# Optimization experiments

Measured on AMD Instinct MI355X. Metric: run time of the kernel, lower is better.

Reference implementation:

```python
import jax, jax.numpy as jnp
import numpy as np

B, T, C = 4, 2048, 1024
NQ, D = 8, C // 8  # n_query heads, head dim = n_embd // 8


def setup_inputs() -> dict:
    key = jax.random.key(0)
    ks = jax.random.split(key, 6)
    s = 0.02
    return {
        "x": jax.random.normal(ks[0], (B, T, C), dtype=jnp.float32),
        "Wk": jax.random.normal(ks[1], (C, D), dtype=jnp.float32) * s,
        "Wv": jax.random.normal(ks[2], (C, D), dtype=jnp.float32) * s,
        "Wq": jax.random.normal(ks[3], (NQ, C, D), dtype=jnp.float32) * s,
        "Wp": jax.random.normal(ks[4], (NQ * D, C), dtype=jnp.float32) * s,
        "bp": jnp.zeros((C,), dtype=jnp.float32),
    }


def reference(x, Wk, Wv, Wq, Wp, bp):
    b, t, c = x.shape
    scale = c ** -0.5  # original scales by n_embd**-0.5, not head-dim
    k = x @ Wk                                   # [B,T,D] shared across heads (MQA)
    v = x @ Wv                                   # [B,T,D]
    q = jnp.einsum("btc,qcd->bqtd", x, Wq)       # [B,NQ,T,D]
    wei = jnp.einsum("bqtd,bsd->bqts", q, k) * scale
    causal = jnp.tril(jnp.ones((t, t), dtype=bool))
    wei = jnp.where(causal, wei, -jnp.inf)
    wei = jax.nn.softmax(wei, axis=-1)
    out = jnp.einsum("bqts,bsd->btqd", wei, v)   # [B,T,NQ,D]
    out = out.reshape(b, t, -1)                  # concat heads -> [B,T,NQ*D]
    return out @ Wp + bp
```

## Files before the change

kernel.cpp:

```cpp
#include <hip/hip_runtime.h>
#include <hip/hip_bf16.h>
#include <cstddef>
#include <cstdint>

#define B 4
#define T 2048
#define C 1024
#define NQ 8
#define D 128
#define M_ROWS (B * T)
#define NTOT (2 * D + NQ * D)

typedef __bf16 bf16x8 __attribute__((ext_vector_type(8)));
typedef float  f32x4  __attribute__((ext_vector_type(4)));

__device__ __forceinline__ ushort f2bf(float f) {
    union { float f; uint32_t u; } v; v.f = f;
    const uint32_t r = (v.u + 0x7fffu + ((v.u >> 16) & 1u)) >> 16;
    return (ushort)r;
}

__device__ __forceinline__ void gld_lds16(const ushort* g, ushort* lds_uniform) {
    __builtin_amdgcn_global_load_lds(
        (const __attribute__((address_space(1))) void*)g,
        (__attribute__((address_space(3))) void*)lds_uniform, 16, 0, 0);
}

__global__ __launch_bounds__(256) void xcvt(const float* __restrict__ x,
                                            ushort* __restrict__ xb) {
    const size_t i = ((size_t)blockIdx.x * 256 + threadIdx.x) * 8;
    const float4 a = *(const float4*)(x + i);
    const float4 b = *(const float4*)(x + i + 4);
    uint4 o;
    o.x = f2bf(a.x) | ((uint32_t)f2bf(a.y) << 16);
    o.y = f2bf(a.z) | ((uint32_t)f2bf(a.w) << 16);
    o.z = f2bf(b.x) | ((uint32_t)f2bf(b.y) << 16);
    o.w = f2bf(b.z) | ((uint32_t)f2bf(b.w) << 16);
    *(uint4*)(xb + i) = o;
}

__device__ __forceinline__ void wtrans_body(const float* __restrict__ src,
                                            ushort* __restrict__ dst, int NC,
                                            int bx, int by) {
    __shared__ ushort Ts[64][72];
    const int tid = threadIdx.x;
    const int k0 = by * 64, c0 = bx * 64;
    {
        const int r = tid >> 2, cq = tid & 3;
#pragma unroll
        for (int i = 0; i < 4; ++i) {
            const int cc = cq * 16 + i * 4;
            const float4 v = *(const float4*)(src + (size_t)(k0 + r) * NC + c0 + cc);
            uint2 o;
            o.x = f2bf(v.x) | ((uint32_t)f2bf(v.y) << 16);
            o.y = f2bf(v.z) | ((uint32_t)f2bf(v.w) << 16);
            *(uint2*)(&Ts[r][cc]) = o;
        }
    }
    __syncthreads();
    {
        const int n = tid >> 2, kq = tid & 3;
        ushort vv[16];
#pragma unroll
        for (int j = 0; j < 16; ++j) vv[j] = Ts[kq * 16 + j][n];
        uint4 o0, o1;
        o0.x = vv[0] | ((uint32_t)vv[1] << 16);  o0.y = vv[2] | ((uint32_t)vv[3] << 16);
        o0.z = vv[4] | ((uint32_t)vv[5] << 16);  o0.w = vv[6] | ((uint32_t)vv[7] << 16);
        o1.x = vv[8] | ((uint32_t)vv[9] << 16);  o1.y = vv[10] | ((uint32_t)vv[11] << 16);
        o1.z = vv[12] | ((uint32_t)vv[13] << 16); o1.w = vv[14] | ((uint32_t)vv[15] << 16);
        ushort* d = dst + (size_t)(c0 + n) * C + k0 + kq * 16;
        *(uint4*)d = o0;
        *(uint4*)(d + 8) = o1;
    }
}

__global__ __launch_bounds__(256) void wtrans_qkv(const float* __restrict__ Wk,
                                                  const float* __restrict__ Wv,
                                                  const float* __restrict__ Wq,
                                                  ushort* __restrict__ WcatT) {
    const int z = blockIdx.z;
    const float* src;
    int rbase;
    if (z == 0)      { src = Wk; rbase = 0; }
    else if (z == 1) { src = Wv; rbase = D; }
    else             { src = Wq + (size_t)(z - 2) * C * D; rbase = 2 * D + (z - 2) * D; }
    wtrans_body(src, WcatT + (size_t)rbase * C, D, blockIdx.x, blockIdx.y);
}

__global__ __launch_bounds__(256) void wtrans_p(const float* __restrict__ Wp,
                                                ushort* __restrict__ WpT) {
    wtrans_body(Wp, WpT, C, blockIdx.x, blockIdx.y);
}

__global__ __launch_bounds__(256) void vtrans(const ushort* __restrict__ qkv,
                                              ushort* __restrict__ vbT) {
    __shared__ ushort Ts[64][136];
    const int tid = threadIdx.x;
    const int kb0 = blockIdx.x * 64;
    {
        const int r = tid >> 2, cq = tid & 3;
        const ushort* src = qkv + (size_t)(kb0 + r) * NTOT + D;
#pragma unroll
        for (int i = 0; i < 4; ++i) {
            const int cc = (cq * 4 + i) * 8;
            *(uint4*)(&Ts[r][cc]) = *(const uint4*)(src + cc);
        }
    }
    __syncthreads();
    {
        const int d = tid >> 1, half = tid & 1;
        ushort vv[32];
#pragma unroll
        for (int k = 0; k < 32; ++k) vv[k] = Ts[half * 32 + k][d];
        uint32_t dw[16];
#pragma unroll
        for (int i = 0; i < 16; ++i) dw[i] = vv[i] | ((uint32_t)vv[16 + i] << 16);
        uint32_t* dst = (uint32_t*)(vbT + (size_t)d * M_ROWS + kb0 + half * 32);
#pragma unroll
        for (int i = 0; i < 4; ++i)
            *(uint4*)(dst + i * 4) = *(uint4*)(&dw[i * 4]);
    }
}

template <bool BF16_OUT>
__global__ __launch_bounds__(256) void gemm_mfma(const ushort* __restrict__ A,
                                                 const ushort* __restrict__ Bt,
                                                 void* __restrict__ Cout,
                                                 const float* __restrict__ bias,
                                                 const int Nout) {
    __shared__ ushort As[128 * 32];
    __shared__ ushort Bs[128 * 32];
    const int tid  = threadIdx.x;
    const int lane = tid & 63;
    const int w    = tid >> 6;
    const int col  = lane & 15;
    const int quad = lane >> 4;
    const int row0 = blockIdx.y * 128;
    const int col0 = blockIdx.x * 128;
    const int wm = w & 1, wn = w >> 1;

    const int srow = lane >> 2;
    const int skk  = (lane & 3) * 8;

    f32x4 acc[4][4];
#pragma unroll
    for (int i = 0; i < 4; ++i)
#pragma unroll
        for (int j = 0; j < 4; ++j) acc[i][j] = (f32x4){0.f, 0.f, 0.f, 0.f};

    for (int k0 = 0; k0 < C; k0 += 32) {
        __syncthreads();
#pragma unroll
        for (int j = 0; j < 2; ++j) {
            const int ci = w * 2 + j;
            const int r  = ci * 16 + srow;
            gld_lds16(A  + (size_t)(row0 + r) * C + k0 + skk, &As[ci * 512]);
            gld_lds16(Bt + (size_t)(col0 + r) * C + k0 + skk, &Bs[ci * 512]);
        }
        __syncthreads();

        bf16x8 af[4], bfr[4];
#pragma unroll
        for (int i = 0; i < 4; ++i)
            af[i] = *(const bf16x8*)&As[(wm * 64 + i * 16 + col) * 32 + quad * 8];
#pragma unroll
        for (int j = 0; j < 4; ++j)
            bfr[j] = *(const bf16x8*)&Bs[(wn * 64 + j * 16 + col) * 32 + quad * 8];
#pragma unroll
        for (int i = 0; i < 4; ++i)
#pragma unroll
            for (int j = 0; j < 4; ++j)
                acc[i][j] = __builtin_amdgcn_mfma_f32_16x16x32_bf16(af[i], bfr[j], acc[i][j], 0, 0, 0);
    }

#pragma unroll
    for (int i = 0; i < 4; ++i) {
#pragma unroll
        for (int r = 0; r < 4; ++r) {
            const int grow = row0 + wm * 64 + i * 16 + quad * 4 + r;
#pragma unroll
            for (int j = 0; j < 4; ++j) {
                const int gcol = col0 + wn * 64 + j * 16 + col;
                const float v = acc[i][j][r];
                if (BF16_OUT) {
                    ((ushort*)Cout)[(size_t)grow * Nout + gcol] = f2bf(v);
                } else {
                    ((float*)Cout)[(size_t)grow * Nout + gcol] = v + bias[gcol];
                }
            }
        }
    }
}

__global__ __launch_bounds__(256) void attn_mfma(const ushort* __restrict__ qkv,
                                                 const ushort* __restrict__ vbT,
                                                 ushort* __restrict__ attb) {
    __shared__ ushort Ks4[4][64][32];
    __shared__ ushort Vt4[4][128][16];
    __shared__ ushort Pt[4][2][16][32];

    const int tid  = threadIdx.x;
    const int lane = tid & 63;
    const int w    = tid >> 6;
    const int col  = lane & 15;
    const int quad = lane >> 4;
    const int h    = blockIdx.y;
    const int b    = blockIdx.z;
    const int qb_i = (b & 1) ? (gridDim.x - 1 - blockIdx.x) : blockIdx.x;
    const int q0   = qb_i * 64;
    const int myq  = q0 + w * 16 + col;

    const ushort* qrow = qkv + (size_t)(b * T + myq) * NTOT + 2 * D + h * D;
    bf16x8 qf[4];
#pragma unroll
    for (int kb2 = 0; kb2 < 4; ++kb2)
        qf[kb2] = *(const bf16x8*)(qrow + kb2 * 32 + quad * 8);

    const ushort* kbase = qkv + (size_t)b * T * NTOT;
    const ushort* vbase = vbT + (size_t)b * T;

    f32x4 O[8];
#pragma unroll
    for (int i = 0; i < 8; ++i) O[i] = (f32x4){0.f, 0.f, 0.f, 0.f};
    float l_r[4] = {0.f, 0.f, 0.f, 0.f};

    const int ntiles = qb_i + 1;
    const int sk_key = lane >> 2;
    const int sk_d   = (lane & 3) * 8;
    const int sv_half = (lane & 1) * 8;

    for (int it = 0; it < ntiles; ++it) {
        const int s0 = it * 64;
        __syncthreads();
#pragma unroll
        for (int kg = 0; kg < 4; ++kg) {
            gld_lds16(kbase + (size_t)(s0 + kg * 16 + sk_key) * NTOT + w * 32 + sk_d,
                      &Ks4[w][kg * 16][0]);
        }
#pragma unroll
        for (int i2 = 0; i2 < 4; ++i2) {
            const int d = (i2 * 64 + lane) >> 1;
            gld_lds16(vbase + (size_t)d * M_ROWS + s0 + w * 16 + sv_half,
                      &Vt4[w][i2 * 32][0]);
        }
        __syncthreads();

        f32x4 S[4];
#pragma unroll
        for (int sub = 0; sub < 4; ++sub) {
            f32x4 a = (f32x4){0.f, 0.f, 0.f, 0.f};
#pragma unroll
            for (int kb2 = 0; kb2 < 4; ++kb2) {
                bf16x8 kf = *(const bf16x8*)(&Ks4[kb2][sub * 16 + col][quad * 8]);
                a = __builtin_amdgcn_mfma_f32_16x16x32_bf16(qf[kb2], kf, a, 0, 0, 0);
            }
            S[sub] = a;
        }

#pragma unroll
        for (int r = 0; r < 4; ++r) {
            const int qq = q0 + w * 16 + quad * 4 + r;
            float p[4];
#pragma unroll
            for (int sub = 0; sub < 4; ++sub) {
                const int key = s0 + sub * 16 + col;
                const float s = (key > qq) ? -1e30f : S[sub][r] * 0.03125f;
                p[sub] = __expf(s);
            }
            l_r[r] += (p[0] + p[1]) + (p[2] + p[3]);
            *(uint32_t*)(&Pt[w][0][quad * 4 + r][col * 2]) =
                f2bf(p[0]) | ((uint32_t)f2bf(p[1]) << 16);
            *(uint32_t*)(&Pt[w][1][quad * 4 + r][col * 2]) =
                f2bf(p[2]) | ((uint32_t)f2bf(p[3]) << 16);
        }

        bf16x8 pa0 = *(const bf16x8*)(&Pt[w][0][col][quad * 8]);
        bf16x8 pa1 = *(const bf16x8*)(&Pt[w][1][col][quad * 8]);
        const int kg0 = quad >> 1;
        const int ko  = (quad & 1) * 8;
#pragma unroll
        for (int nt = 0; nt < 8; ++nt) {
            bf16x8 vf0 = *(const bf16x8*)(&Vt4[kg0][nt * 16 + col][ko]);
            bf16x8 vf1 = *(const bf16x8*)(&Vt4[2 + kg0][nt * 16 + col][ko]);
            O[nt] = __builtin_amdgcn_mfma_f32_16x16x32_bf16(pa0, vf0, O[nt], 0, 0, 0);
            O[nt] = __builtin_amdgcn_mfma_f32_16x16x32_bf16(pa1, vf1, O[nt], 0, 0, 0);
        }
    }

#pragma unroll
    for (int r = 0; r < 4; ++r) {
        float s = l_r[r];
#pragma unroll
        for (int off = 1; off < 16; off <<= 1) s += __shfl_xor(s, off);
        const float inv = 1.0f / s;
        const int t = q0 + w * 16 + quad * 4 + r;
        ushort* orow = attb + (size_t)(b * T + t) * C + h * D;
#pragma unroll
        for (int nt = 0; nt < 8; ++nt) orow[nt * 16 + col] = f2bf(O[nt][r] * inv);
    }
}

extern "C" void kernel_launch(void* const* d_in, const int* in_sizes, int n_in,
                              void* d_out, int out_size, void* d_ws, size_t ws_size,
                              hipStream_t stream) {
    const float* x  = (const float*)d_in[0];
    const float* Wk = (const float*)d_in[1];
    const float* Wv = (const float*)d_in[2];
    const float* Wq = (const float*)d_in[3];
    const float* Wp = (const float*)d_in[4];
    const float* bp = (const float*)d_in[5];
    float* out = (float*)d_out;

    char* ws = (char*)d_ws;
    ushort* xb    = (ushort*)ws;
    ushort* attb  = xb;
    ushort* qkv   = (ushort*)(ws + (size_t)16  * 1024 * 1024);
    ushort* WcatT = (ushort*)(ws + (size_t)36  * 1024 * 1024);
    ushort* WpT   = (ushort*)(ws + (size_t)39  * 1024 * 1024);
    ushort* vbT   = (ushort*)(ws + (size_t)41  * 1024 * 1024);

    xcvt<<<(size_t)M_ROWS * C / (256 * 8), 256, 0, stream>>>(x, xb);
    wtrans_qkv<<<dim3(D / 64, C / 64, 2 + NQ), 256, 0, stream>>>(Wk, Wv, Wq, WcatT);
    wtrans_p<<<dim3(C / 64, C / 64), 256, 0, stream>>>(Wp, WpT);

    gemm_mfma<true><<<dim3(NTOT / 128, M_ROWS / 128), 256, 0, stream>>>(
        xb, WcatT, qkv, nullptr, NTOT);

    vtrans<<<M_ROWS / 64, 256, 0, stream>>>(qkv, vbT);

    attn_mfma<<<dim3(T / 64, NQ, B), 256, 0, stream>>>(qkv, vbT, attb);

    gemm_mfma<false><<<dim3(C / 128, M_ROWS / 128), 256, 0, stream>>>(
        attb, WpT, out, bp, C);
}
```

Measured before the change: 250.5 us.

## Compute transposed scores in attention to keep P in registers, halve block size

The attention kernel now runs 2 waves per block, each owning 32 queries as two 16-row subtiles, which doubles K/V reuse per wave. It computes S transposed (K as the A operand) so the probabilities land in the register layout the PV MFMA expects, which removes the LDS round-trip through Pt. The V transpose kernel permutes keys to match that layout. It also switches to exp2 with a pre-scaled log2e constant, packs with v_cvt_pk_bf16, and applies the causal mask only on the diagonal tile. In exchange, register pressure rises and there are half as many threads per block to issue the K/V loads.

```diff
diff --git a/kernel.cpp b/kernel.cpp
--- a/kernel.cpp
+++ b/kernel.cpp
@@ -13,11 +13,18 @@
 
 typedef __bf16 bf16x8 __attribute__((ext_vector_type(8)));
 typedef float  f32x4  __attribute__((ext_vector_type(4)));
+typedef uint32_t u32x4 __attribute__((ext_vector_type(4)));
 
 __device__ __forceinline__ ushort f2bf(float f) {
     union { float f; uint32_t u; } v; v.f = f;
     const uint32_t r = (v.u + 0x7fffu + ((v.u >> 16) & 1u)) >> 16;
     return (ushort)r;
+}
+
+__device__ __forceinline__ uint32_t cvt_pk_bf16(float lo, float hi) {
+    uint32_t r;
+    asm("v_cvt_pk_bf16_f32 %0, %1, %2" : "=v"(r) : "v"(lo), "v"(hi));
+    return r;
 }
 
 __device__ __forceinline__ void gld_lds16(const ushort* g, ushort* lds_uniform) {
@@ -114,7 +121,12 @@
         for (int k = 0; k < 32; ++k) vv[k] = Ts[half * 32 + k][d];
         uint32_t dw[16];
 #pragma unroll
-        for (int i = 0; i < 16; ++i) dw[i] = vv[i] | ((uint32_t)vv[16 + i] << 16);
+        for (int i = 0; i < 16; ++i) {
+            const int p0 = 2 * i, p1 = 2 * i + 1;
+            const int k0 = (p0 & 3) | (((p0 >> 3) & 3) << 2) | (((p0 >> 2) & 1) << 4);
+            const int k1 = (p1 & 3) | (((p1 >> 3) & 3) << 2) | (((p1 >> 2) & 1) << 4);
+            dw[i] = vv[k0] | ((uint32_t)vv[k1] << 16);
+        }
         uint32_t* dst = (uint32_t*)(vbT + (size_t)d * M_ROWS + kb0 + half * 32);
 #pragma unroll
         for (int i = 0; i < 4; ++i)
@@ -192,12 +204,11 @@
     }
 }
 
-__global__ __launch_bounds__(256) void attn_mfma(const ushort* __restrict__ qkv,
-                                                 const ushort* __restrict__ vbT,
-                                                 ushort* __restrict__ attb) {
+__global__ __launch_bounds__(128, 2) void attn_mfma(const ushort* __restrict__ qkv,
+                                                    const ushort* __restrict__ vbT,
+                                                    ushort* __restrict__ attb) {
     __shared__ ushort Ks4[4][64][32];
     __shared__ ushort Vt4[4][128][16];
-    __shared__ ushort Pt[4][2][16][32];
 
     const int tid  = threadIdx.x;
     const int lane = tid & 63;
@@ -208,95 +219,134 @@
     const int b    = blockIdx.z;
     const int qb_i = (b & 1) ? (gridDim.x - 1 - blockIdx.x) : blockIdx.x;
     const int q0   = qb_i * 64;
-    const int myq  = q0 + w * 16 + col;
-
-    const ushort* qrow = qkv + (size_t)(b * T + myq) * NTOT + 2 * D + h * D;
-    bf16x8 qf[4];
-#pragma unroll
-    for (int kb2 = 0; kb2 < 4; ++kb2)
-        qf[kb2] = *(const bf16x8*)(qrow + kb2 * 32 + quad * 8);
+
+    bf16x8 qf[2][4];
+#pragma unroll
+    for (int qs = 0; qs < 2; ++qs) {
+        const ushort* qrow = qkv + (size_t)(b * T + q0 + w * 32 + qs * 16 + col) * NTOT + 2 * D + h * D;
+#pragma unroll
+        for (int kb2 = 0; kb2 < 4; ++kb2)
+            qf[qs][kb2] = *(const bf16x8*)(qrow + kb2 * 32 + quad * 8);
+    }
 
     const ushort* kbase = qkv + (size_t)b * T * NTOT;
     const ushort* vbase = vbT + (size_t)b * T;
 
-    f32x4 O[8];
-#pragma unroll
-    for (int i = 0; i < 8; ++i) O[i] = (f32x4){0.f, 0.f, 0.f, 0.f};
-    float l_r[4] = {0.f, 0.f, 0.f, 0.f};
-
-    const int ntiles = qb_i + 1;
-    const int sk_key = lane >> 2;
-    const int sk_d   = (lane & 3) * 8;
+    f32x4 O[2][8];
+#pragma unroll
+    for (int qs = 0; qs < 2; ++qs)
+#pragma unroll
+        for (int i = 0; i < 8; ++i) O[qs][i] = (f32x4){0.f, 0.f, 0.f, 0.f};
+    float l_acc[2] = {0.f, 0.f};
+
+    const int ntiles  = qb_i + 1;
+    const int sk_key  = lane >> 2;
+    const int sk_d    = (lane & 3) * 8;
+    const int sv_d    = lane >> 1;
     const int sv_half = (lane & 1) * 8;
+    const int kg0     = quad >> 1;
+    const int ko      = (quad & 1) * 8;
+    const float SC = 0.045084220f;
 
     for (int it = 0; it < ntiles; ++it) {
         const int s0 = it * 64;
         __syncthreads();
 #pragma unroll
-        for (int kg = 0; kg < 4; ++kg) {
-            gld_lds16(kbase + (size_t)(s0 + kg * 16 + sk_key) * NTOT + w * 32 + sk_d,
-                      &Ks4[w][kg * 16][0]);
-        }
-#pragma unroll
-        for (int i2 = 0; i2 < 4; ++i2) {
-            const int d = (i2 * 64 + lane) >> 1;
-            gld_lds16(vbase + (size_t)d * M_ROWS + s0 + w * 16 + sv_half,
-                      &Vt4[w][i2 * 32][0]);
+        for (int cc = 0; cc < 2; ++cc) {
+            const int c = w * 2 + cc;
+#pragma unroll
+            for (int kg = 0; kg < 4; ++kg)
+                gld_lds16(kbase + (size_t)(s0 + kg * 16 + sk_key) * NTOT + c * 32 + sk_d,
+                          &Ks4[c][kg * 16][0]);
+#pragma unroll
+            for (int i2 = 0; i2 < 4; ++i2)
+                gld_lds16(vbase + (size_t)(i2 * 32 + sv_d) * M_ROWS + s0 + c * 16 + sv_half,
+                          &Vt4[c][i2 * 32][0]);
         }
         __syncthreads();
 
-        f32x4 S[4];
+        f32x4 S[2][4];
+#pragma unroll
+        for (int qs = 0; qs < 2; ++qs)
+#pragma unroll
+            for (int sub = 0; sub < 4; ++sub) S[qs][sub] = (f32x4){0.f, 0.f, 0.f, 0.f};
 #pragma unroll
         for (int sub = 0; sub < 4; ++sub) {
-            f32x4 a = (f32x4){0.f, 0.f, 0.f, 0.f};
 #pragma unroll
             for (int kb2 = 0; kb2 < 4; ++kb2) {
                 bf16x8 kf = *(const bf16x8*)(&Ks4[kb2][sub * 16 + col][quad * 8]);
-                a = __builtin_amdgcn_mfma_f32_16x16x32_bf16(qf[kb2], kf, a, 0, 0, 0);
+                S[0][sub] = __builtin_amdgcn_mfma_f32_16x16x32_bf16(kf, qf[0][kb2], S[0][sub], 0, 0, 0);
+                S[1][sub] = __builtin_amdgcn_mfma_f32_16x16x32_bf16(kf, qf[1][kb2], S[1][sub], 0, 0, 0);
             }
-            S[sub] = a;
-        }
-
-#pragma unroll
-        for (int r = 0; r < 4; ++r) {
-            const int qq = q0 + w * 16 + quad * 4 + r;
-            float p[4];
-#pragma unroll
-            for (int sub = 0; sub < 4; ++sub) {
-                const int key = s0 + sub * 16 + col;
-                const float s = (key > qq) ? -1e30f : S[sub][r] * 0.03125f;
-                p[sub] = __expf(s);
+        }
+
+        const bool diag = (it == ntiles - 1);
+        bf16x8 paf[2][2];
+#pragma unroll
+        for (int qs = 0; qs < 2; ++qs) {
+            float p[4][4];
+            if (diag) {
+                const int q = q0 + w * 32 + qs * 16 + col;
+#pragma unroll
+                for (int sub = 0; sub < 4; ++sub)
+#pragma unroll
+                    for (int r = 0; r < 4; ++r) {
+                        const int key = s0 + sub * 16 + quad * 4 + r;
+                        const float sc = (key > q) ? -1e30f : S[qs][sub][r] * SC;
+                        p[sub][r] = __builtin_amdgcn_exp2f(sc);
+                    }
+            } else {
+#pragma unroll
+                for (int sub = 0; sub < 4; ++sub)
+#pragma unroll
+                    for (int r = 0; r < 4; ++r)
+                        p[sub][r] = __builtin_amdgcn_exp2f(S[qs][sub][r] * SC);
             }
-            l_r[r] += (p[0] + p[1]) + (p[2] + p[3]);
-            *(uint32_t*)(&Pt[w][0][quad * 4 + r][col * 2]) =
-                f2bf(p[0]) | ((uint32_t)f2bf(p[1]) << 16);
-            *(uint32_t*)(&Pt[w][1][quad * 4 + r][col * 2]) =
-                f2bf(p[2]) | ((uint32_t)f2bf(p[3]) << 16);
-        }
-
-        bf16x8 pa0 = *(const bf16x8*)(&Pt[w][0][col][quad * 8]);
-        bf16x8 pa1 = *(const bf16x8*)(&Pt[w][1][col][quad * 8]);
-        const int kg0 = quad >> 1;
-        const int ko  = (quad & 1) * 8;
+            float ls = 0.f;
+#pragma unroll
+            for (int sub = 0; sub < 4; ++sub)
+                ls += (p[sub][0] + p[sub][1]) + (p[sub][2] + p[sub][3]);
+            l_acc[qs] += ls;
+
+            u32x4 w0, w1;
+            w0.x = cvt_pk_bf16(p[0][0], p[0][1]);
+            w0.y = cvt_pk_bf16(p[0][2], p[0][3]);
+            w0.z = cvt_pk_bf16(p[1][0], p[1][1]);
+            w0.w = cvt_pk_bf16(p[1][2], p[1][3]);
+            w1.x = cvt_pk_bf16(p[2][0], p[2][1]);
+            w1.y = cvt_pk_bf16(p[2][2], p[2][3]);
+            w1.z = cvt_pk_bf16(p[3][0], p[3][1]);
+            w1.w = cvt_pk_bf16(p[3][2], p[3][3]);
+            paf[qs][0] = __builtin_bit_cast(bf16x8, w0);
+            paf[qs][1] = __builtin_bit_cast(bf16x8, w1);
+        }
+
 #pragma unroll
         for (int nt = 0; nt < 8; ++nt) {
             bf16x8 vf0 = *(const bf16x8*)(&Vt4[kg0][nt * 16 + col][ko]);
             bf16x8 vf1 = *(const bf16x8*)(&Vt4[2 + kg0][nt * 16 + col][ko]);
-            O[nt] = __builtin_amdgcn_mfma_f32_16x16x32_bf16(pa0, vf0, O[nt], 0, 0, 0);
-            O[nt] = __builtin_amdgcn_mfma_f32_16x16x32_bf16(pa1, vf1, O[nt], 0, 0, 0);
-        }
-    }
-
-#pragma unroll
-    for (int r = 0; r < 4; ++r) {
-        float s = l_r[r];
-#pragma unroll
-        for (int off = 1; off < 16; off <<= 1) s += __shfl_xor(s, off);
-        const float inv = 1.0f / s;
-        const int t = q0 + w * 16 + quad * 4 + r;
-        ushort* orow = attb + (size_t)(b * T + t) * C + h * D;
-#pragma unroll
-        for (int nt = 0; nt < 8; ++nt) orow[nt * 16 + col] = f2bf(O[nt][r] * inv);
+#pragma unroll
+            for (int qs = 0; qs < 2; ++qs) {
+                O[qs][nt] = __builtin_amdgcn_mfma_f32_16x16x32_bf16(paf[qs][0], vf0, O[qs][nt], 0, 0, 0);
+                O[qs][nt] = __builtin_amdgcn_mfma_f32_16x16x32_bf16(paf[qs][1], vf1, O[qs][nt], 0, 0, 0);
+            }
+        }
+    }
+
+#pragma unroll
+    for (int qs = 0; qs < 2; ++qs) {
+        float s = l_acc[qs];
+        s += __shfl_xor(s, 16);
+        s += __shfl_xor(s, 32);
+#pragma unroll
+        for (int r = 0; r < 4; ++r) {
+            const float inv = 1.0f / __shfl(s, quad * 4 + r);
+            const int t = q0 + w * 32 + qs * 16 + quad * 4 + r;
+            ushort* orow = attb + (size_t)(b * T + t) * C + h * D;
+#pragma unroll
+            for (int nt = 0; nt < 8; ++nt)
+                orow[nt * 16 + col] = f2bf(O[qs][nt][r] * inv);
+        }
     }
 }
 
@@ -328,7 +378,7 @@
 
     vtrans<<<M_ROWS / 64, 256, 0, stream>>>(qkv, vbT);
 
-    attn_mfma<<<dim3(T / 64, NQ, B), 256, 0, stream>>>(qkv, vbT, attb);
+    attn_mfma<<<dim3(T / 64, NQ, B), 128, 0, stream>>>(qkv, vbT, attb);
 
     gemm_mfma<false><<<dim3(C / 128, M_ROWS / 128), 256, 0, stream>>>(
         attb, WpT, out, bp, C);
```

Measured after the change: 227.7 us. 9.1% less time.
